# Optimization experiments

Hardware: AMD Instinct MI355X
Metric: run time of the kernel (lower is better)

## Reference

```python
import jax, jax.numpy as jnp
import numpy as np

B, S, E, H = 4, 2048, 1024, 16
DH = E // H  # 64
ROPE_THETA = 10000.0


def _rope(x):
    # x: [B, H, S, DH]; llama-style rotate-half RoPE over full head dim
    half = DH // 2
    inv_freq = 1.0 / (ROPE_THETA ** (jnp.arange(0, half, dtype=jnp.float32) * 2.0 / DH))
    ang = jnp.arange(S, dtype=jnp.float32)[:, None] * inv_freq[None, :]  # [S, half]
    cos = jnp.concatenate([jnp.cos(ang), jnp.cos(ang)], axis=-1)  # [S, DH]
    sin = jnp.concatenate([jnp.sin(ang), jnp.sin(ang)], axis=-1)
    x1, x2 = x[..., :half], x[..., half:]
    rot = jnp.concatenate([-x2, x1], axis=-1)
    return x * cos[None, None] + rot * sin[None, None]


def setup_inputs() -> dict:
    key = jax.random.key(0)
    ks = jax.random.split(key, 8)
    std = 1.0 / np.sqrt(E)
    X = jax.random.normal(ks[0], (B, S, E), dtype=jnp.float32)
    Wq = jax.random.normal(ks[1], (E, E), dtype=jnp.float32) * std
    Wk = jax.random.normal(ks[2], (E, E), dtype=jnp.float32) * std
    Wv = jax.random.normal(ks[3], (E, E), dtype=jnp.float32) * std
    Wo = jax.random.normal(ks[4], (E, E), dtype=jnp.float32) * std
    bq = jnp.zeros((E,), jnp.float32)
    bk = jnp.zeros((E,), jnp.float32)
    bv = jnp.zeros((E,), jnp.float32)
    bo = jnp.zeros((E,), jnp.float32)
    curr_seq_lens = jax.random.randint(ks[5], (B,), S // 2, S + 1, dtype=jnp.int32)
    return {"X": X, "Wq": Wq, "bq": bq, "Wk": Wk, "bk": bk, "Wv": Wv, "bv": bv,
            "Wo": Wo, "bo": bo, "curr_seq_lens": curr_seq_lens}


def reference(X, Wq, bq, Wk, bk, Wv, bv, Wo, bo, curr_seq_lens):
    # projections (torch Linear: y = x @ W.T + b); dropout is identity (p=0 / eval)
    q = X @ Wq.T + bq
    k = X @ Wk.T + bk
    v = X @ Wv.T + bv
    # [B, S, E] -> [B, H, S, DH]
    to_heads = lambda t: t.reshape(B, S, H, DH).transpose(0, 2, 1, 3)
    q, k, v = to_heads(q), to_heads(k), to_heads(v)
    q = _rope(q)
    k = _rope(k)
    # varlen causal attention: key j visible to query i iff j <= i and j < len[b] (and i < len[b])
    scale = 1.0 / np.sqrt(DH)
    scores = jnp.einsum('bhqd,bhkd->bhqk', q, k) * scale
    pos = jnp.arange(S)
    causal = pos[:, None] >= pos[None, :]                       # [S, S]
    valid_k = pos[None, :] < curr_seq_lens[:, None, None]       # [B, 1, S] after broadcast
    mask = causal[None, None] & valid_k[:, None]                # [B, 1, S, S]
    scores = jnp.where(mask, scores, jnp.float32(-1e30))
    attn = jax.nn.softmax(scores, axis=-1)
    out = jnp.einsum('bhqk,bhkd->bhqd', attn, v)
    # zero out rows for padded queries (kernel only writes valid rows)
    valid_q = (pos[None, :] < curr_seq_lens[:, None])[:, None, :, None]  # [B,1,S,1]
    out = jnp.where(valid_q, out, 0.0)
    out = out.transpose(0, 2, 1, 3).reshape(B, S, E)
    return out @ Wo.T + bo
```

## Files before the change

kernel.cpp:

```cpp
#include <hip/hip_runtime.h>

typedef __bf16 bf16;
typedef __bf16 bf16x4_t __attribute__((ext_vector_type(4)));
typedef __bf16 bf16x8_t __attribute__((ext_vector_type(8)));
typedef float  f32x4_t  __attribute__((ext_vector_type(4)));
typedef float  f32x16_t __attribute__((ext_vector_type(16)));
typedef unsigned int u32x4_t __attribute__((ext_vector_type(4)));

#define S_LEN 2048
#define NHEAD 16
#define NBH   64

static __device__ __forceinline__ void glds16(const void* g, void* l) {
  __builtin_amdgcn_global_load_lds(
      (const __attribute__((address_space(1))) unsigned int*)g,
      (__attribute__((address_space(3))) unsigned int*)l, 16, 0, 0);
}

static __device__ __forceinline__ unsigned pk2(float lo, float hi) {
  unsigned short a = __builtin_bit_cast(unsigned short, (bf16)lo);
  unsigned short b = __builtin_bit_cast(unsigned short, (bf16)hi);
  return (unsigned)a | ((unsigned)b << 16);
}

__global__ __launch_bounds__(256) void cvt_x_kernel(const float4* __restrict__ in,
                                                    bf16x4_t* __restrict__ out) {
  int i = blockIdx.x * 256 + threadIdx.x;
  float4 v = in[i];
  bf16x4_t o = { (bf16)v.x, (bf16)v.y, (bf16)v.z, (bf16)v.w };
  out[i] = o;
}

__global__ __launch_bounds__(256) void cvt_w_kernel(const float* __restrict__ w0, const float* __restrict__ w1,
                                                    const float* __restrict__ w2, const float* __restrict__ w3,
                                                    bf16x4_t* __restrict__ out) {
  int i = blockIdx.x * 256 + threadIdx.x;
  int sel = i >> 18;
  int j = i & 262143;
  const float4* src = (const float4*)(sel == 0 ? w0 : sel == 1 ? w1 : sel == 2 ? w2 : w3);
  float4 v = src[j];
  bf16x4_t o = { (bf16)v.x, (bf16)v.y, (bf16)v.z, (bf16)v.w };
  out[i] = o;
}

template<int MODE>
__global__ __launch_bounds__(256) void gemm_bt_kernel(
    const bf16* __restrict__ A, const bf16* __restrict__ Wb,
    const float* __restrict__ bias0, const float* __restrict__ bias1, const float* __restrict__ bias2,
    bf16* __restrict__ q_ws, bf16* __restrict__ k_ws, bf16* __restrict__ v_t,
    float* __restrict__ dout)
{
  __shared__ __align__(16) bf16 As[128 * 32];
  __shared__ __align__(16) bf16 Bs[128 * 32];
  const int tid  = threadIdx.x;
  const int lane = tid & 63, wid = tid >> 6;
  const int ql = lane & 15, lg = lane >> 4;
  const int wm = wid >> 1, wn = wid & 1;
  const int bm = blockIdx.x, bn = blockIdx.y;
  const int z  = (MODE == 0) ? blockIdx.z : 0;

  const bf16* Ag = A  + (long)bm * 128 * 1024;
  const bf16* Bg = Wb + (long)z * 1024 * 1024 + (long)bn * 128 * 1024;

  f32x4_t acc[4][4];
  const f32x4_t zero4 = { 0.f, 0.f, 0.f, 0.f };
  #pragma unroll
  for (int i = 0; i < 4; i++)
    #pragma unroll
    for (int j = 0; j < 4; j++) acc[i][j] = zero4;

  for (int k0 = 0; k0 < 1024; k0 += 32) {
    __syncthreads();
    #pragma unroll
    for (int r = 0; r < 2; r++) {
      int tt = tid + r * 256;
      int row = tt >> 2, kc = (tt & 3) * 8;
      glds16(Ag + (long)row * 1024 + k0 + kc, (void*)&As[tt * 8]);
    }
    #pragma unroll
    for (int r = 0; r < 2; r++) {
      int tt = tid + r * 256;
      int row = tt >> 2, kc = (tt & 3) * 8;
      glds16(Bg + (long)row * 1024 + k0 + kc, (void*)&Bs[tt * 8]);
    }
    __syncthreads();

    bf16x8_t af[4], bf_[4];
    #pragma unroll
    for (int m = 0; m < 4; m++) af[m]  = *(const bf16x8_t*)&As[(wm * 64 + m * 16 + ql) * 32 + lg * 8];
    #pragma unroll
    for (int n = 0; n < 4; n++) bf_[n] = *(const bf16x8_t*)&Bs[(wn * 64 + n * 16 + ql) * 32 + lg * 8];
    #pragma unroll
    for (int m = 0; m < 4; m++)
      #pragma unroll
      for (int n = 0; n < 4; n++)
        acc[m][n] = __builtin_amdgcn_mfma_f32_16x16x32_bf16(af[m], bf_[n], acc[m][n], 0, 0, 0);
  }

  if (MODE == 1) {
    #pragma unroll
    for (int m = 0; m < 4; m++) {
      int rb = bm * 128 + wm * 64 + m * 16 + lg * 4;
      #pragma unroll
      for (int n = 0; n < 4; n++) {
        int colg = bn * 128 + wn * 64 + n * 16 + ql;
        float bb = bias0[colg];
        #pragma unroll
        for (int r = 0; r < 4; r++)
          dout[(long)(rb + r) * 1024 + colg] = acc[m][n][r] + bb;
      }
    }
  } else if (z == 2) {
    #pragma unroll
    for (int m = 0; m < 4; m++) {
      int rb = bm * 128 + wm * 64 + m * 16 + lg * 4;
      int bb_ = rb >> 11;
      int s0  = rb & 2047;
      int kc  = s0 >> 4;
      int c   = (s0 >> 2) & 3;
      int hi_ = c & 1, b2_ = c >> 1;
      #pragma unroll
      for (int n = 0; n < 4; n++) {
        int colg = bn * 128 + wn * 64 + n * 16 + ql;
        int h = colg >> 6, d = colg & 63;
        float bb = bias2[colg];
        int dblk = d >> 5, lq_ = d & 31;
        long idx = ((((long)(bb_ * NHEAD + h) * 128 + kc) * 2 + dblk) * 64 + hi_ * 32 + lq_) * 8 + 4 * b2_;
        ushort4 pkt;
        pkt.x = __builtin_bit_cast(unsigned short, (bf16)(acc[m][n][0] + bb));
        pkt.y = __builtin_bit_cast(unsigned short, (bf16)(acc[m][n][1] + bb));
        pkt.z = __builtin_bit_cast(unsigned short, (bf16)(acc[m][n][2] + bb));
        pkt.w = __builtin_bit_cast(unsigned short, (bf16)(acc[m][n][3] + bb));
        *(ushort4*)&v_t[idx] = pkt;
      }
    }
  } else if (z == 1) {
    #pragma unroll
    for (int m = 0; m < 4; m++) {
      int rb = bm * 128 + wm * 64 + m * 16 + lg * 4;
      int bb_ = rb >> 11;
      int s0  = rb & 2047;
      #pragma unroll
      for (int n = 0; n < 2; n++) {
        int colg = bn * 128 + wn * 64 + n * 16 + ql;
        int h = colg >> 6, d = colg & 63;
        float b1 = bias1[colg], b2 = bias1[colg + 32];
        float inv = exp2f((float)d * -0.41524101186092026f);
        int ds_ = d >> 4, hi_ = (d >> 3) & 1, j_ = d & 7;
        long base_bh = (long)(bb_ * NHEAD + h) * 64;
        #pragma unroll
        for (int r = 0; r < 4; r++) {
          int s = s0 + r;
          float ang = (float)s * inv;
          float sn, cs;
          __sincosf(ang, &sn, &cs);
          float x1 = acc[m][n][r] + b1;
          float x2 = acc[m][n + 2][r] + b2;
          int kb = s >> 5, lq_ = s & 31;
          long lbase = ((base_bh + kb) * 4 + ds_) * 64 + hi_ * 32 + lq_;
          k_ws[lbase * 8 + j_]       = (bf16)(x1 * cs - x2 * sn);
          k_ws[(lbase + 128) * 8 + j_] = (bf16)(x2 * cs + x1 * sn);
        }
      }
    }
  } else {
    #pragma unroll
    for (int m = 0; m < 4; m++) {
      int rb = bm * 128 + wm * 64 + m * 16 + lg * 4;
      int bb_ = rb >> 11;
      int s0  = rb & 2047;
      #pragma unroll
      for (int n = 0; n < 2; n++) {
        int colg = bn * 128 + wn * 64 + n * 16 + ql;
        int h = colg >> 6, d = colg & 63;
        float b1 = bias0[colg], b2 = bias0[colg + 32];
        float inv = exp2f((float)d * -0.41524101186092026f);
        #pragma unroll
        for (int r = 0; r < 4; r++) {
          int s = s0 + r;
          float ang = (float)s * inv;
          float sn, cs;
          __sincosf(ang, &sn, &cs);
          float x1 = acc[m][n][r] + b1;
          float x2 = acc[m][n + 2][r] + b2;
          long base = ((long)(bb_ * NHEAD + h) * S_LEN + s) * 64;
          q_ws[base + d]      = (bf16)(x1 * cs - x2 * sn);
          q_ws[base + d + 32] = (bf16)(x2 * cs + x1 * sn);
        }
      }
    }
  }
}

__global__ __launch_bounds__(64, 4) void attn_kernel(const bf16* __restrict__ qw, const bf16* __restrict__ kfr_,
                                                     const bf16* __restrict__ vfr_, bf16* __restrict__ ow,
                                                     const int* __restrict__ lens)
{
  const int lane = threadIdx.x & 63;
  const int lq = lane & 31, hi = lane >> 5;
  const int bh = blockIdx.x, b = bh >> 4, h = bh & 15;
  const int len = lens[b];
  const int tile = 63 - (int)blockIdx.y;
  const int q0 = tile * 32;
  const int qg = q0 + lq;

  const bf16* qh  = qw   + (long)bh * S_LEN * 64;
  const bf16* kfr = kfr_ + (long)bh * (64 * 4 * 64 * 8);
  const bf16* vfr = vfr_ + (long)bh * (128 * 2 * 64 * 8);
  bf16* obase = ow + ((long)b * S_LEN + qg) * 1024 + h * 64;

  if (q0 >= len) {
    ushort4 zz; zz.x = zz.y = zz.z = zz.w = 0;
    #pragma unroll
    for (int dblk = 0; dblk < 2; dblk++)
      #pragma unroll
      for (int g = 0; g < 4; g++)
        *(ushort4*)&obase[dblk * 32 + g * 8 + hi * 4] = zz;
    return;
  }

  bf16x8_t qf[4];
  #pragma unroll
  for (int ds = 0; ds < 4; ds++)
    qf[ds] = *(const bf16x8_t*)&qh[(long)qg * 64 + ds * 16 + hi * 8];

  f32x16_t o0, o1;
  #pragma unroll
  for (int r = 0; r < 16; r++) { o0[r] = 0.f; o1[r] = 0.f; }

  const float SCL = 0.125f * 1.44269504088896f;
  const float THR = 11.5415603f;
  float m_run = -1e30f, l_run = 0.f;
  const int kend = min(q0 + 31, len - 1);

  bf16x8_t kf[4];
  #pragma unroll
  for (int ds = 0; ds < 4; ds++)
    kf[ds] = *(const bf16x8_t*)&kfr[((long)ds * 64 + lane) * 8];

  for (int k0 = 0; k0 <= kend; k0 += 32) {
    const int kc = k0 >> 4;
    bf16x8_t vw[2][2];
    #pragma unroll
    for (int dblk = 0; dblk < 2; dblk++)
      #pragma unroll
      for (int ks = 0; ks < 2; ks++)
        vw[dblk][ks] = *(const bf16x8_t*)&vfr[(((long)(kc + ks) * 2 + dblk) * 64 + lane) * 8];

    f32x16_t s;
    #pragma unroll
    for (int r = 0; r < 16; r++) s[r] = 0.f;
    #pragma unroll
    for (int ds = 0; ds < 4; ds++)
      s = __builtin_amdgcn_mfma_f32_32x32x16_bf16(kf[ds], qf[ds], s, 0, 0, 0);

    if (k0 + 32 <= kend) {
      const long nb = (long)((k0 >> 5) + 1) * 4;
      #pragma unroll
      for (int ds = 0; ds < 4; ds++)
        kf[ds] = *(const bf16x8_t*)&kfr[((nb + ds) * 64 + lane) * 8];
    }

    if (!(k0 < q0 && k0 + 32 <= len)) {
      #pragma unroll
      for (int r = 0; r < 16; r++) {
        int kg = k0 + (r & 3) + 8 * (r >> 2) + 4 * hi;
        s[r] = (kg <= qg && kg < len) ? s[r] : -3.0e38f;
      }
    }

    float mx = s[0];
    #pragma unroll
    for (int r = 1; r < 16; r++) mx = fmaxf(mx, s[r]);
    mx = fmaxf(mx, __shfl_xor(mx, 32));
    float mxl = mx * SCL;

    if (__any(mxl > m_run + THR)) {
      float m_new = fmaxf(m_run, mxl);
      float sc = __builtin_amdgcn_exp2f(m_run - m_new);
      l_run *= sc;
      #pragma unroll
      for (int r = 0; r < 16; r++) { o0[r] *= sc; o1[r] *= sc; }
      m_run = m_new;
    }

    float pv[16];
    float ps = 0.f;
    #pragma unroll
    for (int r = 0; r < 16; r++) {
      pv[r] = __builtin_amdgcn_exp2f(__builtin_fmaf(s[r], SCL, -m_run));
      ps += pv[r];
    }
    ps += __shfl_xor(ps, 32);
    l_run += ps;

    u32x4_t f0, f1;
    f0.x = pk2(pv[0],  pv[1]);  f0.y = pk2(pv[2],  pv[3]);
    f0.z = pk2(pv[4],  pv[5]);  f0.w = pk2(pv[6],  pv[7]);
    f1.x = pk2(pv[8],  pv[9]);  f1.y = pk2(pv[10], pv[11]);
    f1.z = pk2(pv[12], pv[13]); f1.w = pk2(pv[14], pv[15]);
    bf16x8_t pf0 = __builtin_bit_cast(bf16x8_t, f0);
    bf16x8_t pf1 = __builtin_bit_cast(bf16x8_t, f1);

    o0 = __builtin_amdgcn_mfma_f32_32x32x16_bf16(vw[0][0], pf0, o0, 0, 0, 0);
    o1 = __builtin_amdgcn_mfma_f32_32x32x16_bf16(vw[1][0], pf0, o1, 0, 0, 0);
    o0 = __builtin_amdgcn_mfma_f32_32x32x16_bf16(vw[0][1], pf1, o0, 0, 0, 0);
    o1 = __builtin_amdgcn_mfma_f32_32x32x16_bf16(vw[1][1], pf1, o1, 0, 0, 0);
  }

  float rinv = (qg < len) ? (1.0f / l_run) : 0.f;
  #pragma unroll
  for (int g = 0; g < 4; g++) {
    ushort4 p0, p1;
    p0.x = __builtin_bit_cast(unsigned short, (bf16)(o0[4 * g + 0] * rinv));
    p0.y = __builtin_bit_cast(unsigned short, (bf16)(o0[4 * g + 1] * rinv));
    p0.z = __builtin_bit_cast(unsigned short, (bf16)(o0[4 * g + 2] * rinv));
    p0.w = __builtin_bit_cast(unsigned short, (bf16)(o0[4 * g + 3] * rinv));
    p1.x = __builtin_bit_cast(unsigned short, (bf16)(o1[4 * g + 0] * rinv));
    p1.y = __builtin_bit_cast(unsigned short, (bf16)(o1[4 * g + 1] * rinv));
    p1.z = __builtin_bit_cast(unsigned short, (bf16)(o1[4 * g + 2] * rinv));
    p1.w = __builtin_bit_cast(unsigned short, (bf16)(o1[4 * g + 3] * rinv));
    *(ushort4*)&obase[g * 8 + hi * 4]      = p0;
    *(ushort4*)&obase[32 + g * 8 + hi * 4] = p1;
  }
}

extern "C" void kernel_launch(void* const* d_in, const int* in_sizes, int n_in,
                              void* d_out, int out_size, void* d_ws, size_t ws_size,
                              hipStream_t stream)
{
  const float* X  = (const float*)d_in[0];
  const float* Wq = (const float*)d_in[1];
  const float* bq = (const float*)d_in[2];
  const float* Wk = (const float*)d_in[3];
  const float* bk = (const float*)d_in[4];
  const float* Wv = (const float*)d_in[5];
  const float* bv = (const float*)d_in[6];
  const float* Wo = (const float*)d_in[7];
  const float* bo = (const float*)d_in[8];
  const int* lens = (const int*)d_in[9];
  float* out = (float*)d_out;

  char* ws = (char*)d_ws;
  bf16* x_bf = (bf16*)(ws);
  bf16* w_bf = (bf16*)(ws + (16u << 20));
  bf16* q_ws = (bf16*)(ws + (24u << 20));
  bf16* kfrag = (bf16*)(ws + (40u << 20));
  bf16* vfrag = (bf16*)(ws + (56u << 20));
  bf16* o_ws = (bf16*)(ws + (72u << 20));

  cvt_x_kernel<<<8192, 256, 0, stream>>>((const float4*)X, (bf16x4_t*)x_bf);
  cvt_w_kernel<<<4096, 256, 0, stream>>>(Wq, Wk, Wv, Wo, (bf16x4_t*)w_bf);
  gemm_bt_kernel<0><<<dim3(64, 8, 3), 256, 0, stream>>>(x_bf, w_bf, bq, bk, bv,
                                                        q_ws, kfrag, vfrag, nullptr);
  attn_kernel<<<dim3(NBH, 64), 64, 0, stream>>>(q_ws, kfrag, vfrag, o_ws, lens);
  gemm_bt_kernel<1><<<dim3(64, 8, 1), 256, 0, stream>>>(o_ws, w_bf + 3u * 1048576u, bo, bo, bo,
                                                        q_ws, kfrag, vfrag, out);
}
```

Before: 240.1 us.

## Split attention KV loop across four waves with LDS softmax merge

Each attention block now runs four wavefronts, and each wave handles every fourth 32-key chunk for the same 32-query tile. Partial outputs, running maxima and sums from waves 1-3 go to shared memory, and wave 0 merges them with rescaling before normalising and writing. This shortens the serial per-tile loop and adds parallelism for long causal rows, which should help load imbalance. The cost is LDS use, a block barrier, merge work, and idle waves on short tiles.

```diff
diff --git a/kernel.cpp b/kernel.cpp
--- a/kernel.cpp
+++ b/kernel.cpp
@@ -192,11 +192,12 @@
   }
 }
 
-__global__ __launch_bounds__(64, 4) void attn_kernel(const bf16* __restrict__ qw, const bf16* __restrict__ kfr_,
-                                                     const bf16* __restrict__ vfr_, bf16* __restrict__ ow,
-                                                     const int* __restrict__ lens)
+__global__ __launch_bounds__(256, 4) void attn_kernel(const bf16* __restrict__ qw, const bf16* __restrict__ kfr_,
+                                                      const bf16* __restrict__ vfr_, bf16* __restrict__ ow,
+                                                      const int* __restrict__ lens)
 {
-  const int lane = threadIdx.x & 63;
+  const int tid = threadIdx.x;
+  const int lane = tid & 63, wid = tid >> 6;
   const int lq = lane & 31, hi = lane >> 5;
   const int bh = blockIdx.x, b = bh >> 4, h = bh & 15;
   const int len = lens[b];
@@ -204,18 +205,24 @@
   const int q0 = tile * 32;
   const int qg = q0 + lq;
 
+  __shared__ float sm_o[3][64][33];
+  __shared__ float sm_m[3][64];
+  __shared__ float sm_l[3][64];
+
   const bf16* qh  = qw   + (long)bh * S_LEN * 64;
   const bf16* kfr = kfr_ + (long)bh * (64 * 4 * 64 * 8);
   const bf16* vfr = vfr_ + (long)bh * (128 * 2 * 64 * 8);
   bf16* obase = ow + ((long)b * S_LEN + qg) * 1024 + h * 64;
 
   if (q0 >= len) {
-    ushort4 zz; zz.x = zz.y = zz.z = zz.w = 0;
-    #pragma unroll
-    for (int dblk = 0; dblk < 2; dblk++)
-      #pragma unroll
-      for (int g = 0; g < 4; g++)
-        *(ushort4*)&obase[dblk * 32 + g * 8 + hi * 4] = zz;
+    if (wid == 0) {
+      ushort4 zz; zz.x = zz.y = zz.z = zz.w = 0;
+      #pragma unroll
+      for (int dblk = 0; dblk < 2; dblk++)
+        #pragma unroll
+        for (int g = 0; g < 4; g++)
+          *(ushort4*)&obase[dblk * 32 + g * 8 + hi * 4] = zz;
+    }
     return;
   }
 
@@ -236,9 +243,9 @@
   bf16x8_t kf[4];
   #pragma unroll
   for (int ds = 0; ds < 4; ds++)
-    kf[ds] = *(const bf16x8_t*)&kfr[((long)ds * 64 + lane) * 8];
-
-  for (int k0 = 0; k0 <= kend; k0 += 32) {
+    kf[ds] = *(const bf16x8_t*)&kfr[(((long)wid * 4 + ds) * 64 + lane) * 8];
+
+  for (int k0 = wid * 32; k0 <= kend; k0 += 128) {
     const int kc = k0 >> 4;
     bf16x8_t vw[2][2];
     #pragma unroll
@@ -254,8 +261,8 @@
     for (int ds = 0; ds < 4; ds++)
       s = __builtin_amdgcn_mfma_f32_32x32x16_bf16(kf[ds], qf[ds], s, 0, 0, 0);
 
-    if (k0 + 32 <= kend) {
-      const long nb = (long)((k0 >> 5) + 1) * 4;
+    if (k0 + 128 <= kend) {
+      const long nb = (long)((k0 >> 5) + 4) * 4;
       #pragma unroll
       for (int ds = 0; ds < 4; ds++)
         kf[ds] = *(const bf16x8_t*)&kfr[((nb + ds) * 64 + lane) * 8];
@@ -308,20 +315,49 @@
     o1 = __builtin_amdgcn_mfma_f32_32x32x16_bf16(vw[1][1], pf1, o1, 0, 0, 0);
   }
 
-  float rinv = (qg < len) ? (1.0f / l_run) : 0.f;
-  #pragma unroll
-  for (int g = 0; g < 4; g++) {
-    ushort4 p0, p1;
-    p0.x = __builtin_bit_cast(unsigned short, (bf16)(o0[4 * g + 0] * rinv));
-    p0.y = __builtin_bit_cast(unsigned short, (bf16)(o0[4 * g + 1] * rinv));
-    p0.z = __builtin_bit_cast(unsigned short, (bf16)(o0[4 * g + 2] * rinv));
-    p0.w = __builtin_bit_cast(unsigned short, (bf16)(o0[4 * g + 3] * rinv));
-    p1.x = __builtin_bit_cast(unsigned short, (bf16)(o1[4 * g + 0] * rinv));
-    p1.y = __builtin_bit_cast(unsigned short, (bf16)(o1[4 * g + 1] * rinv));
-    p1.z = __builtin_bit_cast(unsigned short, (bf16)(o1[4 * g + 2] * rinv));
-    p1.w = __builtin_bit_cast(unsigned short, (bf16)(o1[4 * g + 3] * rinv));
-    *(ushort4*)&obase[g * 8 + hi * 4]      = p0;
-    *(ushort4*)&obase[32 + g * 8 + hi * 4] = p1;
+  if (wid != 0) {
+    #pragma unroll
+    for (int r = 0; r < 16; r++) {
+      sm_o[wid - 1][lane][r]      = o0[r];
+      sm_o[wid - 1][lane][16 + r] = o1[r];
+    }
+    sm_m[wid - 1][lane] = m_run;
+    sm_l[wid - 1][lane] = l_run;
+  }
+  __syncthreads();
+  if (wid == 0) {
+    float M = m_run;
+    #pragma unroll
+    for (int w = 0; w < 3; w++) M = fmaxf(M, sm_m[w][lane]);
+    float sc0 = __builtin_amdgcn_exp2f(m_run - M);
+    float lt = l_run * sc0;
+    #pragma unroll
+    for (int r = 0; r < 16; r++) { o0[r] *= sc0; o1[r] *= sc0; }
+    #pragma unroll
+    for (int w = 0; w < 3; w++) {
+      float scw = __builtin_amdgcn_exp2f(sm_m[w][lane] - M);
+      lt += sm_l[w][lane] * scw;
+      #pragma unroll
+      for (int r = 0; r < 16; r++) {
+        o0[r] += sm_o[w][lane][r]      * scw;
+        o1[r] += sm_o[w][lane][16 + r] * scw;
+      }
+    }
+    float rinv = (qg < len) ? (1.0f / lt) : 0.f;
+    #pragma unroll
+    for (int g = 0; g < 4; g++) {
+      ushort4 p0, p1;
+      p0.x = __builtin_bit_cast(unsigned short, (bf16)(o0[4 * g + 0] * rinv));
+      p0.y = __builtin_bit_cast(unsigned short, (bf16)(o0[4 * g + 1] * rinv));
+      p0.z = __builtin_bit_cast(unsigned short, (bf16)(o0[4 * g + 2] * rinv));
+      p0.w = __builtin_bit_cast(unsigned short, (bf16)(o0[4 * g + 3] * rinv));
+      p1.x = __builtin_bit_cast(unsigned short, (bf16)(o1[4 * g + 0] * rinv));
+      p1.y = __builtin_bit_cast(unsigned short, (bf16)(o1[4 * g + 1] * rinv));
+      p1.z = __builtin_bit_cast(unsigned short, (bf16)(o1[4 * g + 2] * rinv));
+      p1.w = __builtin_bit_cast(unsigned short, (bf16)(o1[4 * g + 3] * rinv));
+      *(ushort4*)&obase[g * 8 + hi * 4]      = p0;
+      *(ushort4*)&obase[32 + g * 8 + hi * 4] = p1;
+    }
   }
 }
 
@@ -353,7 +389,7 @@
   cvt_w_kernel<<<4096, 256, 0, stream>>>(Wq, Wk, Wv, Wo, (bf16x4_t*)w_bf);
   gemm_bt_kernel<0><<<dim3(64, 8, 3), 256, 0, stream>>>(x_bf, w_bf, bq, bk, bv,
                                                         q_ws, kfrag, vfrag, nullptr);
-  attn_kernel<<<dim3(NBH, 64), 64, 0, stream>>>(q_ws, kfrag, vfrag, o_ws, lens);
+  attn_kernel<<<dim3(NBH, 64), 256, 0, stream>>>(q_ws, kfrag, vfrag, o_ws, lens);
   gemm_bt_kernel<1><<<dim3(64, 8, 1), 256, 0, stream>>>(o_ws, w_bf + 3u * 1048576u, bo, bo, bo,
                                                         q_ws, kfrag, vfrag, out);
 }
```

New measurement: 240.0 us. No clear change (-0.1%).
